# Performance work log

Measured on AMD Instinct MI355X. Metric: run time of the kernel, lower is better.

Reference implementation:

```python
import jax, jax.numpy as jnp
import numpy as np

B, T, F, L = 8, 2048, 64, 48  # batch, time, numFilters, attentionLen


def setup_inputs() -> dict:
    key = jax.random.key(0)
    k1, k2 = jax.random.split(key)
    he = jax.random.normal(k1, (B, T, F), dtype=jnp.float32)
    # DecoderBlock modeled as a Dense(numFilters) producing the per-step query
    W = jax.random.normal(k2, (F, F), dtype=jnp.float32) / jnp.sqrt(jnp.float32(F))
    b = jnp.zeros((F,), dtype=jnp.float32)
    return {"he": he, "W": W, "b": b}


def reference(he, W, b):
    # he: [B, T, F]. Query at step i: q_i = he[:, i] @ W + b.
    # Window for step i>=1: he[:, max(i-L, 0):i, :]; step 0 attends to he[:, 0, :].
    Bb, Tt, Ff = he.shape
    q = jnp.einsum('btf,fg->btg', he, W) + b            # [B, T, F]

    i = jnp.arange(Tt)[:, None]                          # [T, 1]
    k = jnp.arange(L)[None, :]                           # [1, L]
    rel = i - L + k                                      # window position j = i-L+k (so j in [i-L, i-1])
    valid = jnp.where(i == 0, k == L - 1, rel >= 0)      # step 0: only position 0 (last slot)
    idx = jnp.clip(rel, 0, Tt - 1)                       # [T, L]

    he_win = he[:, idx, :]                               # [B, T, L, F] gathered sliding windows
    scores = jnp.einsum('btlf,btf->btl', he_win, q)      # [B, T, L]
    scores = jnp.where(valid[None], scores, jnp.float32(-1e30))
    w = jax.nn.softmax(scores, axis=-1)                  # softmax over the window (axis=1 in original)
    ctx = jnp.einsum('btl,btlf->btf', w, he_win)         # [B, T, F]
    return ctx
```

## Files before the change

### kernel.cpp

```cpp
#include <hip/hip_runtime.h>
#include <hip/hip_bf16.h>

#define BB 8
#define TT 2048
#define FF 64
#define LL 48
#define TB 32
#define RE (TB + LL)
#define NW 8
#define NT (NW * 64)

typedef __attribute__((ext_vector_type(8))) short bf16x8;
typedef __attribute__((ext_vector_type(4))) float f32x4;

#define HE_HI 0
#define HE_LO 10240
#define WT_HI 20480
#define WT_LO 28672
#define QQ_HI 36864
#define QQ_LO 40960
#define HET   20480
#define PT    36864
#define RED   45056
#define SMEM_BYTES 46080

__device__ __forceinline__ unsigned short f2b(float x) {
    unsigned int u = __builtin_bit_cast(unsigned int, x);
    return (unsigned short)((u + 0x7FFFu + ((u >> 16) & 1u)) >> 16);
}
__device__ __forceinline__ float b2f(unsigned short h) {
    return __builtin_bit_cast(float, (unsigned int)h << 16);
}

__global__ __launch_bounds__(NT, 2)
void ContextBlock_kernel(const float* __restrict__ he,
                         const float* __restrict__ Wm,
                         const float* __restrict__ bias,
                         float* __restrict__ out)
{
    __shared__ __align__(16) unsigned char smem[SMEM_BYTES];

    const int tid  = threadIdx.x;
    const int wave = tid >> 6;
    const int lane = tid & 63;
    const int bb   = blockIdx.y;
    const int t0   = blockIdx.x * TB;

    const float* heb = he + (size_t)bb * TT * FF;

    const float4* he4 = (const float4*)heb;
    for (int e = tid; e < RE * 16; e += NT) {
        int r = e >> 4, c4 = e & 15;
        int g = t0 - LL + r; g = g < 0 ? 0 : g;
        float4 v = he4[g * 16 + c4];
        unsigned short h0 = f2b(v.x), h1 = f2b(v.y), h2 = f2b(v.z), h3 = f2b(v.w);
        unsigned short l0 = f2b(v.x - b2f(h0)), l1 = f2b(v.y - b2f(h1));
        unsigned short l2 = f2b(v.z - b2f(h2)), l3 = f2b(v.w - b2f(h3));
        unsigned long long pkh = (unsigned long long)h0 | ((unsigned long long)h1 << 16)
                               | ((unsigned long long)h2 << 32) | ((unsigned long long)h3 << 48);
        unsigned long long pkl = (unsigned long long)l0 | ((unsigned long long)l1 << 16)
                               | ((unsigned long long)l2 << 32) | ((unsigned long long)l3 << 48);
        int off = r * 128 + ((((c4 >> 1) ^ (r & 7)) << 4)) + ((c4 & 1) << 3);
        *(unsigned long long*)(smem + HE_HI + off) = pkh;
        *(unsigned long long*)(smem + HE_LO + off) = pkl;
    }
    const float4* w4 = (const float4*)Wm;
    for (int e = tid; e < 1024; e += NT) {
        int f = e >> 4, g4 = e & 15;
        float4 v = w4[e];
        float vv[4] = {v.x, v.y, v.z, v.w};
        #pragma unroll
        for (int i = 0; i < 4; ++i) {
            int g = g4 * 4 + i;
            unsigned short hi = f2b(vv[i]);
            unsigned short lo = f2b(vv[i] - b2f(hi));
            int off = g * 128 + ((((f >> 3) ^ (g & 7)) << 4)) + ((f & 7) << 1);
            *(unsigned short*)(smem + WT_HI + off) = hi;
            *(unsigned short*)(smem + WT_LO + off) = lo;
        }
    }
    __syncthreads();

    const int l15 = lane & 15;
    const int lhi = lane >> 4;

    {
        int mt = wave >> 2, nt = wave & 3;
        f32x4 acc = (f32x4){0.f, 0.f, 0.f, 0.f};
        int arow = LL + mt * 16 + l15;
        int colg = nt * 16 + l15;
        #pragma unroll
        for (int kf = 0; kf < 2; ++kf) {
            int chunk = 4 * kf + lhi;
            int offA = arow * 128 + ((chunk ^ (arow & 7)) << 4);
            int offB = colg * 128 + ((chunk ^ (colg & 7)) << 4);
            bf16x8 ah = *(const bf16x8*)(smem + HE_HI + offA);
            bf16x8 al = *(const bf16x8*)(smem + HE_LO + offA);
            bf16x8 bh = *(const bf16x8*)(smem + WT_HI + offB);
            bf16x8 bl = *(const bf16x8*)(smem + WT_LO + offB);
            acc = __builtin_amdgcn_mfma_f32_16x16x32_bf16(ah, bh, acc, 0, 0, 0);
            acc = __builtin_amdgcn_mfma_f32_16x16x32_bf16(ah, bl, acc, 0, 0, 0);
            acc = __builtin_amdgcn_mfma_f32_16x16x32_bf16(al, bh, acc, 0, 0, 0);
        }
        float bv = bias[colg];
        #pragma unroll
        for (int i = 0; i < 4; ++i) {
            int tok = mt * 16 + lhi * 4 + i;
            float qv = acc[i] + bv;
            unsigned short hi = f2b(qv);
            unsigned short lo = f2b(qv - b2f(hi));
            int off = tok * 128 + ((((colg >> 3) ^ (tok & 7)) << 4)) + ((colg & 7) << 1);
            *(unsigned short*)(smem + QQ_HI + off) = hi;
            *(unsigned short*)(smem + QQ_LO + off) = lo;
        }
    }
    __syncthreads();

    const int ct = wave >> 2, uu = wave & 3;
    const int rt = ct + uu;
    const int tok = ct * 16 + l15;
    f32x4 sc;
    {
        f32x4 acc = (f32x4){0.f, 0.f, 0.f, 0.f};
        int arow = rt * 16 + l15;
        #pragma unroll
        for (int kf = 0; kf < 2; ++kf) {
            int chunk = 4 * kf + lhi;
            int offA = arow * 128 + ((chunk ^ (arow & 7)) << 4);
            int offB = tok * 128 + ((chunk ^ (tok & 7)) << 4);
            bf16x8 ah = *(const bf16x8*)(smem + HE_HI + offA);
            bf16x8 al = *(const bf16x8*)(smem + HE_LO + offA);
            bf16x8 bh = *(const bf16x8*)(smem + QQ_HI + offB);
            bf16x8 bl = *(const bf16x8*)(smem + QQ_LO + offB);
            acc = __builtin_amdgcn_mfma_f32_16x16x32_bf16(ah, bh, acc, 0, 0, 0);
            acc = __builtin_amdgcn_mfma_f32_16x16x32_bf16(ah, bl, acc, 0, 0, 0);
            acc = __builtin_amdgcn_mfma_f32_16x16x32_bf16(al, bh, acc, 0, 0, 0);
        }
        sc = acc;
    }
    float m = -1e30f;
    #pragma unroll
    for (int i = 0; i < 4; ++i) {
        int r_ext = rt * 16 + lhi * 4 + i;
        int l = r_ext - tok;
        bool valid = (t0 == 0 && tok == 0) ? (r_ext == LL - 1)
                                           : (l >= 0 && l < LL && (t0 + r_ext) >= LL);
        float s = valid ? sc[i] : -1e30f;
        sc[i] = s;
        m = fmaxf(m, s);
    }
    m = fmaxf(m, __shfl_xor(m, 16));
    m = fmaxf(m, __shfl_xor(m, 32));
    float sum = 0.f;
    #pragma unroll
    for (int i = 0; i < 4; ++i)
        sum += __expf(sc[i] - m);
    sum += __shfl_xor(sum, 16);
    sum += __shfl_xor(sum, 32);
    if (lane < 16)
        *(float2*)(smem + RED + tok * 32 + uu * 8) = make_float2(m, sum);
    __syncthreads();

    {
        float M = -1e30f;
        float2 p[4];
        #pragma unroll
        for (int u = 0; u < 4; ++u) {
            p[u] = *(const float2*)(smem + RED + tok * 32 + u * 8);
            M = fmaxf(M, p[u].x);
        }
        float T = 0.f;
        #pragma unroll
        for (int u = 0; u < 4; ++u)
            T += p[u].y * __expf(p[u].x - M);
        float invT = 1.0f / T;
        int rbase = rt * 16 + lhi * 4;
        unsigned short w0 = f2b(__expf(sc[0] - M) * invT);
        unsigned short w1 = f2b(__expf(sc[1] - M) * invT);
        unsigned short w2 = f2b(__expf(sc[2] - M) * invT);
        unsigned short w3 = f2b(__expf(sc[3] - M) * invT);
        unsigned long long pk = (unsigned long long)w0 | ((unsigned long long)w1 << 16)
                              | ((unsigned long long)w2 << 32) | ((unsigned long long)w3 << 48);
        *(unsigned long long*)(smem + PT + tok * 256
            + ((((rbase >> 3) ^ (tok & 7)) << 4)) + ((rbase & 7) << 1)) = pk;
        int zbase = (((rt + 4) & 7) * 16) + lhi * 4;
        *(unsigned long long*)(smem + PT + tok * 256
            + ((((zbase >> 3) ^ (tok & 7)) << 4)) + ((zbase & 7) << 1)) = 0ull;
    }
    for (int e = tid; e < RE * 64; e += NT) {
        int r = e >> 6, f = e & 63;
        unsigned short h = *(const unsigned short*)
            (smem + HE_HI + r * 128 + ((((f >> 3) ^ (r & 7)) << 4)) + ((f & 7) << 1));
        *(unsigned short*)
            (smem + HET + f * 256 + ((((r >> 3) ^ (f & 7)) << 4)) + ((r & 7) << 1)) = h;
    }
    __syncthreads();

    {
        int mt = wave >> 2, nt = wave & 3;
        f32x4 acc = (f32x4){0.f, 0.f, 0.f, 0.f};
        int arow = mt * 16 + l15;
        int brow = nt * 16 + l15;
        #pragma unroll
        for (int kk = 0; kk < 2; ++kk) {
            int chunk = 2 * mt + 4 * kk + lhi;
            bf16x8 a  = *(const bf16x8*)(smem + PT  + arow * 256 + ((chunk ^ (arow & 7)) << 4));
            bf16x8 bo = *(const bf16x8*)(smem + HET + brow * 256 + ((chunk ^ (brow & 7)) << 4));
            acc = __builtin_amdgcn_mfma_f32_16x16x32_bf16(a, bo, acc, 0, 0, 0);
        }
        #pragma unroll
        for (int i = 0; i < 4; ++i) {
            int tk = mt * 16 + lhi * 4 + i;
            out[((size_t)bb * TT + t0 + tk) * FF + nt * 16 + l15] = acc[i];
        }
    }
}

extern "C" void kernel_launch(void* const* d_in, const int* in_sizes, int n_in,
                              void* d_out, int out_size, void* d_ws, size_t ws_size,
                              hipStream_t stream) {
    const float* he   = (const float*)d_in[0];
    const float* Wm   = (const float*)d_in[1];
    const float* bias = (const float*)d_in[2];
    float* out        = (float*)d_out;

    dim3 grid(TT / TB, BB);
    ContextBlock_kernel<<<grid, NT, 0, stream>>>(he, Wm, bias, out);
}
```

Baseline: 12.32 us.

## Double token tile, drop W and HE-transpose staging, compute softmax per wave

Doubles the tokens per block from 32 to 64, so the 48-row window halo is loaded and converted relative to more work. W is no longer staged in shared memory: each lane reads its W column straight from global memory and splits it into hi/lo bf16 parts in registers. The explicit HE transpose buffer is replaced by strided 2-byte shared-memory gathers for the PV operand. Four waves now each compute a full 64-wide score row and its softmax, which removes the cross-wave max/sum reduction and one barrier. The cost is half as many blocks in the grid, idle waves during the score phase, uncoalesced global W reads, and many scalar shared-memory loads.

```diff
diff --git a/kernel.cpp b/kernel.cpp
--- a/kernel.cpp
+++ b/kernel.cpp
@@ -5,7 +5,7 @@
 #define TT 2048
 #define FF 64
 #define LL 48
-#define TB 32
+#define TB 64
 #define RE (TB + LL)
 #define NW 8
 #define NT (NW * 64)
@@ -14,15 +14,11 @@
 typedef __attribute__((ext_vector_type(4))) float f32x4;
 
 #define HE_HI 0
-#define HE_LO 10240
-#define WT_HI 20480
-#define WT_LO 28672
-#define QQ_HI 36864
-#define QQ_LO 40960
-#define HET   20480
-#define PT    36864
-#define RED   45056
-#define SMEM_BYTES 46080
+#define HE_LO 14336
+#define QQ_HI 28672
+#define QQ_LO 36864
+#define PT    45056
+#define SMEM_BYTES 53248
 
 __device__ __forceinline__ unsigned short f2b(float x) {
     unsigned int u = __builtin_bit_cast(unsigned int, x);
@@ -32,7 +28,7 @@
     return __builtin_bit_cast(float, (unsigned int)h << 16);
 }
 
-__global__ __launch_bounds__(NT, 2)
+__global__ __launch_bounds__(NT, 4)
 void ContextBlock_kernel(const float* __restrict__ he,
                          const float* __restrict__ Wm,
                          const float* __restrict__ bias,
@@ -64,28 +60,15 @@
         *(unsigned long long*)(smem + HE_HI + off) = pkh;
         *(unsigned long long*)(smem + HE_LO + off) = pkl;
     }
-    const float4* w4 = (const float4*)Wm;
-    for (int e = tid; e < 1024; e += NT) {
-        int f = e >> 4, g4 = e & 15;
-        float4 v = w4[e];
-        float vv[4] = {v.x, v.y, v.z, v.w};
-        #pragma unroll
-        for (int i = 0; i < 4; ++i) {
-            int g = g4 * 4 + i;
-            unsigned short hi = f2b(vv[i]);
-            unsigned short lo = f2b(vv[i] - b2f(hi));
-            int off = g * 128 + ((((f >> 3) ^ (g & 7)) << 4)) + ((f & 7) << 1);
-            *(unsigned short*)(smem + WT_HI + off) = hi;
-            *(unsigned short*)(smem + WT_LO + off) = lo;
-        }
-    }
     __syncthreads();
 
     const int l15 = lane & 15;
     const int lhi = lane >> 4;
 
-    {
-        int mt = wave >> 2, nt = wave & 3;
+    #pragma unroll
+    for (int s = 0; s < 2; ++s) {
+        int q = wave * 2 + s;
+        int mt = q >> 2, nt = q & 3;
         f32x4 acc = (f32x4){0.f, 0.f, 0.f, 0.f};
         int arow = LL + mt * 16 + l15;
         int colg = nt * 16 + l15;
@@ -93,11 +76,16 @@
         for (int kf = 0; kf < 2; ++kf) {
             int chunk = 4 * kf + lhi;
             int offA = arow * 128 + ((chunk ^ (arow & 7)) << 4);
-            int offB = colg * 128 + ((chunk ^ (colg & 7)) << 4);
             bf16x8 ah = *(const bf16x8*)(smem + HE_HI + offA);
             bf16x8 al = *(const bf16x8*)(smem + HE_LO + offA);
-            bf16x8 bh = *(const bf16x8*)(smem + WT_HI + offB);
-            bf16x8 bl = *(const bf16x8*)(smem + WT_LO + offB);
+            bf16x8 bh, bl;
+            #pragma unroll
+            for (int j = 0; j < 8; ++j) {
+                float wv = Wm[(kf * 32 + lhi * 8 + j) * FF + colg];
+                unsigned short hh = f2b(wv);
+                bh[j] = (short)hh;
+                bl[j] = (short)f2b(wv - b2f(hh));
+            }
             acc = __builtin_amdgcn_mfma_f32_16x16x32_bf16(ah, bh, acc, 0, 0, 0);
             acc = __builtin_amdgcn_mfma_f32_16x16x32_bf16(ah, bl, acc, 0, 0, 0);
             acc = __builtin_amdgcn_mfma_f32_16x16x32_bf16(al, bh, acc, 0, 0, 0);
@@ -116,102 +104,93 @@
     }
     __syncthreads();
 
-    const int ct = wave >> 2, uu = wave & 3;
-    const int rt = ct + uu;
-    const int tok = ct * 16 + l15;
-    f32x4 sc;
-    {
+    if (wave < 4) {
+        const int ct   = wave;
+        const int tokc = ct * 16 + l15;
+        float sc[4][4];
+        float m = -1e30f;
+        #pragma unroll
+        for (int u = 0; u < 4; ++u) {
+            int arow = (ct + u) * 16 + l15;
+            f32x4 acc = (f32x4){0.f, 0.f, 0.f, 0.f};
+            #pragma unroll
+            for (int kf = 0; kf < 2; ++kf) {
+                int chunk = 4 * kf + lhi;
+                int offA = arow * 128 + ((chunk ^ (arow & 7)) << 4);
+                int offB = tokc * 128 + ((chunk ^ (tokc & 7)) << 4);
+                bf16x8 ah = *(const bf16x8*)(smem + HE_HI + offA);
+                bf16x8 al = *(const bf16x8*)(smem + HE_LO + offA);
+                bf16x8 bh = *(const bf16x8*)(smem + QQ_HI + offB);
+                bf16x8 bl = *(const bf16x8*)(smem + QQ_LO + offB);
+                acc = __builtin_amdgcn_mfma_f32_16x16x32_bf16(ah, bh, acc, 0, 0, 0);
+                acc = __builtin_amdgcn_mfma_f32_16x16x32_bf16(ah, bl, acc, 0, 0, 0);
+                acc = __builtin_amdgcn_mfma_f32_16x16x32_bf16(al, bh, acc, 0, 0, 0);
+            }
+            #pragma unroll
+            for (int i = 0; i < 4; ++i) {
+                int r_ext = (ct + u) * 16 + lhi * 4 + i;
+                int l = r_ext - tokc;
+                bool valid = (t0 == 0 && tokc == 0) ? (r_ext == LL - 1)
+                                                    : (l >= 0 && l < LL && (t0 + r_ext) >= LL);
+                float sv = valid ? acc[i] : -1e30f;
+                sc[u][i] = sv;
+                m = fmaxf(m, sv);
+            }
+        }
+        m = fmaxf(m, __shfl_xor(m, 16));
+        m = fmaxf(m, __shfl_xor(m, 32));
+        float sum = 0.f;
+        #pragma unroll
+        for (int u = 0; u < 4; ++u)
+            #pragma unroll
+            for (int i = 0; i < 4; ++i) {
+                float p = __expf(sc[u][i] - m);
+                sc[u][i] = p;
+                sum += p;
+            }
+        sum += __shfl_xor(sum, 16);
+        sum += __shfl_xor(sum, 32);
+        float invT = 1.0f / sum;
+        #pragma unroll
+        for (int u = 0; u < 4; ++u) {
+            unsigned short w0 = f2b(sc[u][0] * invT);
+            unsigned short w1 = f2b(sc[u][1] * invT);
+            unsigned short w2 = f2b(sc[u][2] * invT);
+            unsigned short w3 = f2b(sc[u][3] * invT);
+            unsigned long long pk = (unsigned long long)w0 | ((unsigned long long)w1 << 16)
+                                  | ((unsigned long long)w2 << 32) | ((unsigned long long)w3 << 48);
+            int c = 2 * u + (lhi >> 1);
+            *(unsigned long long*)(smem + PT + tokc * 128
+                + ((c ^ (tokc & 7)) << 4) + ((lhi & 1) << 3)) = pk;
+        }
+    }
+    __syncthreads();
+
+    #pragma unroll
+    for (int s2 = 0; s2 < 2; ++s2) {
+        int q = wave * 2 + s2;
+        int mt = q >> 2, nt = q & 3;
+        int tokrow = mt * 16 + l15;
+        int fcol   = nt * 16 + l15;
         f32x4 acc = (f32x4){0.f, 0.f, 0.f, 0.f};
-        int arow = rt * 16 + l15;
-        #pragma unroll
-        for (int kf = 0; kf < 2; ++kf) {
-            int chunk = 4 * kf + lhi;
-            int offA = arow * 128 + ((chunk ^ (arow & 7)) << 4);
-            int offB = tok * 128 + ((chunk ^ (tok & 7)) << 4);
-            bf16x8 ah = *(const bf16x8*)(smem + HE_HI + offA);
-            bf16x8 al = *(const bf16x8*)(smem + HE_LO + offA);
-            bf16x8 bh = *(const bf16x8*)(smem + QQ_HI + offB);
-            bf16x8 bl = *(const bf16x8*)(smem + QQ_LO + offB);
-            acc = __builtin_amdgcn_mfma_f32_16x16x32_bf16(ah, bh, acc, 0, 0, 0);
-            acc = __builtin_amdgcn_mfma_f32_16x16x32_bf16(ah, bl, acc, 0, 0, 0);
-            acc = __builtin_amdgcn_mfma_f32_16x16x32_bf16(al, bh, acc, 0, 0, 0);
-        }
-        sc = acc;
-    }
-    float m = -1e30f;
-    #pragma unroll
-    for (int i = 0; i < 4; ++i) {
-        int r_ext = rt * 16 + lhi * 4 + i;
-        int l = r_ext - tok;
-        bool valid = (t0 == 0 && tok == 0) ? (r_ext == LL - 1)
-                                           : (l >= 0 && l < LL && (t0 + r_ext) >= LL);
-        float s = valid ? sc[i] : -1e30f;
-        sc[i] = s;
-        m = fmaxf(m, s);
-    }
-    m = fmaxf(m, __shfl_xor(m, 16));
-    m = fmaxf(m, __shfl_xor(m, 32));
-    float sum = 0.f;
-    #pragma unroll
-    for (int i = 0; i < 4; ++i)
-        sum += __expf(sc[i] - m);
-    sum += __shfl_xor(sum, 16);
-    sum += __shfl_xor(sum, 32);
-    if (lane < 16)
-        *(float2*)(smem + RED + tok * 32 + uu * 8) = make_float2(m, sum);
-    __syncthreads();
-
-    {
-        float M = -1e30f;
-        float2 p[4];
-        #pragma unroll
-        for (int u = 0; u < 4; ++u) {
-            p[u] = *(const float2*)(smem + RED + tok * 32 + u * 8);
-            M = fmaxf(M, p[u].x);
-        }
-        float T = 0.f;
-        #pragma unroll
-        for (int u = 0; u < 4; ++u)
-            T += p[u].y * __expf(p[u].x - M);
-        float invT = 1.0f / T;
-        int rbase = rt * 16 + lhi * 4;
-        unsigned short w0 = f2b(__expf(sc[0] - M) * invT);
-        unsigned short w1 = f2b(__expf(sc[1] - M) * invT);
-        unsigned short w2 = f2b(__expf(sc[2] - M) * invT);
-        unsigned short w3 = f2b(__expf(sc[3] - M) * invT);
-        unsigned long long pk = (unsigned long long)w0 | ((unsigned long long)w1 << 16)
-                              | ((unsigned long long)w2 << 32) | ((unsigned long long)w3 << 48);
-        *(unsigned long long*)(smem + PT + tok * 256
-            + ((((rbase >> 3) ^ (tok & 7)) << 4)) + ((rbase & 7) << 1)) = pk;
-        int zbase = (((rt + 4) & 7) * 16) + lhi * 4;
-        *(unsigned long long*)(smem + PT + tok * 256
-            + ((((zbase >> 3) ^ (tok & 7)) << 4)) + ((zbase & 7) << 1)) = 0ull;
-    }
-    for (int e = tid; e < RE * 64; e += NT) {
-        int r = e >> 6, f = e & 63;
-        unsigned short h = *(const unsigned short*)
-            (smem + HE_HI + r * 128 + ((((f >> 3) ^ (r & 7)) << 4)) + ((f & 7) << 1));
-        *(unsigned short*)
-            (smem + HET + f * 256 + ((((r >> 3) ^ (f & 7)) << 4)) + ((r & 7) << 1)) = h;
-    }
-    __syncthreads();
-
-    {
-        int mt = wave >> 2, nt = wave & 3;
-        f32x4 acc = (f32x4){0.f, 0.f, 0.f, 0.f};
-        int arow = mt * 16 + l15;
-        int brow = nt * 16 + l15;
         #pragma unroll
         for (int kk = 0; kk < 2; ++kk) {
-            int chunk = 2 * mt + 4 * kk + lhi;
-            bf16x8 a  = *(const bf16x8*)(smem + PT  + arow * 256 + ((chunk ^ (arow & 7)) << 4));
-            bf16x8 bo = *(const bf16x8*)(smem + HET + brow * 256 + ((chunk ^ (brow & 7)) << 4));
-            acc = __builtin_amdgcn_mfma_f32_16x16x32_bf16(a, bo, acc, 0, 0, 0);
+            int cA = kk * 4 + lhi;
+            bf16x8 a = *(const bf16x8*)(smem + PT + tokrow * 128
+                + ((cA ^ (tokrow & 7)) << 4));
+            bf16x8 b;
+            #pragma unroll
+            for (int j = 0; j < 8; ++j) {
+                int r = mt * 16 + kk * 32 + lhi * 8 + j;
+                b[j] = *(const short*)(smem + HE_HI + r * 128
+                    + ((((fcol >> 3) ^ (r & 7)) << 4)) + ((fcol & 7) << 1));
+            }
+            acc = __builtin_amdgcn_mfma_f32_16x16x32_bf16(a, b, acc, 0, 0, 0);
         }
         #pragma unroll
         for (int i = 0; i < 4; ++i) {
             int tk = mt * 16 + lhi * 4 + i;
-            out[((size_t)bb * TT + t0 + tk) * FF + nt * 16 + l15] = acc[i];
+            out[((size_t)bb * TT + t0 + tk) * FF + fcol] = acc[i];
         }
     }
 }
```

Result: faster. 11.19 us (-9.2%).
